# Performance work log

Measured on AMD Instinct MI355X. Metric: run time of the kernel, lower is better.

## Reference

```python
import jax, jax.numpy as jnp
import numpy as np

N_EMBED = 1024
HEAD_SIZE = 64


def setup_inputs() -> dict:
    key = jax.random.key(0)
    kx, kk, kq, kv = jax.random.split(key, 4)
    B, T = 8, 2048
    x = jax.random.normal(kx, (B, T, N_EMBED), dtype=jnp.float32)
    # nn.Linear weights, stored as (in, out) so projection is x @ W
    s = 1.0 / np.sqrt(N_EMBED)
    Wk = jax.random.uniform(kk, (N_EMBED, HEAD_SIZE), jnp.float32, -s, s)
    Wq = jax.random.uniform(kq, (N_EMBED, HEAD_SIZE), jnp.float32, -s, s)
    Wv = jax.random.uniform(kv, (N_EMBED, HEAD_SIZE), jnp.float32, -s, s)
    return {"x": x, "Wk": Wk, "Wq": Wq, "Wv": Wv}


def reference(x, Wk, Wq, Wv):
    # x: [B, T, C] with C = n_embed
    C = x.shape[-1]
    k = x @ Wk  # [B, T, H]
    q = x @ Wq  # [B, T, H]
    v = x @ Wv  # [B, T, H]
    # NOTE: original scales by n_embed**-0.5, not head_size**-0.5
    wei = jnp.einsum("bth,bsh->bts", q, k) * (C ** -0.5)  # [B, T, T]
    wei = jax.nn.softmax(wei, axis=-1)
    # dropout = 0.0 (eval mode) -> identity
    out = jnp.einsum("bts,bsh->bth", wei, v)  # [B, T, H]
    return out
```

## Files before the change

kernel.cpp:

```cpp
#include <hip/hip_runtime.h>
#include <stdint.h>


#define B_ 8
#define T_ 2048
#define C_ 1024
#define H_ 64

typedef float f32x4 __attribute__((ext_vector_type(4)));
typedef short s16x8 __attribute__((ext_vector_type(8)));

__device__ __forceinline__ unsigned int rhu16(float f) {
    return (__float_as_uint(f) + 0x8000u) >> 16;
}
__device__ __forceinline__ unsigned int pkbf(float lo, float hi) {
    unsigned int a = __float_as_uint(lo) + 0x8000u;
    unsigned int b = __float_as_uint(hi) + 0x8000u;
    return __builtin_amdgcn_perm(b, a, 0x07060302u);
}

__global__ __launch_bounds__(256) void wconv(const float* __restrict__ Wk,
        const float* __restrict__ Wq, const float* __restrict__ Wv,
        unsigned short* __restrict__ Wt) {
    int col = blockIdx.x;
    int mat = col >> 6, h = col & 63;
    const float* W = (mat == 0) ? Wk : ((mat == 1) ? Wq : Wv);
    float sc = (mat == 1) ? 0.03125f : 1.0f;
    for (int c = threadIdx.x; c < C_; c += 256)
        Wt[col * C_ + c] = (unsigned short)rhu16(W[c * H_ + h] * sc);
}

__global__ __launch_bounds__(256, 2) void qkv(const float* __restrict__ x,
        const unsigned short* __restrict__ Wt,
        unsigned short* __restrict__ kb, unsigned short* __restrict__ qb,
        unsigned short* __restrict__ vtb) {
    __shared__ unsigned short Ws[192 * 72];

    const int t = threadIdx.x, lane = t & 63, w = t >> 6;
    const int l15 = lane & 15, quad = lane >> 4;
    const int bx = blockIdx.x;
    const int bb = bx >> 6;
    const int mt = ((bx & 7) << 3) | ((bx >> 3) & 7);
    const int m0 = bb * T_ + mt * 32;
    const int colb = w * 48;

    f32x4 acc[2][3];
    #pragma unroll
    for (int rt = 0; rt < 2; rt++)
        #pragma unroll
        for (int ct = 0; ct < 3; ct++)
            #pragma unroll
            for (int j = 0; j < 4; j++) acc[rt][ct][j] = 0.0f;

    for (int c0 = 0; c0 < C_; c0 += 64) {
        __syncthreads();
        #pragma unroll
        for (int u0 = 0; u0 < 6; u0++) {
            int u = t + (u0 << 8);
            int cl = u >> 3, co = (u & 7) << 3;
            uint4 d = *reinterpret_cast<const uint4*>(&Wt[cl * C_ + c0 + co]);
            *reinterpret_cast<uint4*>(&Ws[cl * 72 + co]) = d;
        }
        __syncthreads();
        s16x8 af[2][2];
        #pragma unroll
        for (int rt = 0; rt < 2; rt++)
            #pragma unroll
            for (int ks = 0; ks < 2; ks++) {
                const float* xp = &x[(size_t)(m0 + rt * 16 + l15) * C_ + c0 + ks * 32 + quad * 8];
                float4 a = *reinterpret_cast<const float4*>(xp);
                float4 b = *reinterpret_cast<const float4*>(xp + 4);
                uint4 pk;
                pk.x = pkbf(a.x, a.y); pk.y = pkbf(a.z, a.w);
                pk.z = pkbf(b.x, b.y); pk.w = pkbf(b.z, b.w);
                af[rt][ks] = *reinterpret_cast<s16x8*>(&pk);
            }
        #pragma unroll
        for (int ks = 0; ks < 2; ks++) {
            s16x8 bfr[3];
            #pragma unroll
            for (int ct = 0; ct < 3; ct++)
                bfr[ct] = *reinterpret_cast<const s16x8*>(
                    &Ws[(colb + ct * 16 + l15) * 72 + ks * 32 + quad * 8]);
            #pragma unroll
            for (int rt = 0; rt < 2; rt++)
                #pragma unroll
                for (int ct = 0; ct < 3; ct++)
                    acc[rt][ct] = __builtin_amdgcn_mfma_f32_16x16x32_bf16(
                        af[rt][ks], bfr[ct], acc[rt][ct], 0, 0, 0);
        }
    }
    #pragma unroll
    for (int ct = 0; ct < 3; ct++) {
        int cb = colb + ct * 16;
        int sel = cb >> 6;
        int h = (cb & 63) + l15;
        #pragma unroll
        for (int rt = 0; rt < 2; rt++) {
            int row0 = m0 + rt * 16 + quad * 4;
            if (sel < 2) {
                unsigned short* dst = sel ? qb : kb;
                #pragma unroll
                for (int r = 0; r < 4; r++)
                    dst[(size_t)(row0 + r) * H_ + h] = (unsigned short)rhu16(acc[rt][ct][r]);
            } else {
                int tt = row0 - bb * T_;
                uint2 pk;
                pk.x = pkbf(acc[rt][ct][0], acc[rt][ct][1]);
                pk.y = pkbf(acc[rt][ct][2], acc[rt][ct][3]);
                *reinterpret_cast<uint2*>(&vtb[((size_t)bb * H_ + h) * T_ + tt]) = pk;
            }
        }
    }
}

__global__ __launch_bounds__(256, 2) void attn(
        const unsigned short* __restrict__ qb,
        const unsigned short* __restrict__ kb,
        const unsigned short* __restrict__ vtb,
        float* __restrict__ out) {
    __shared__ float smemf[6432];

    const int t = threadIdx.x, lane = t & 63, w = t >> 6;
    const int l15 = lane & 15, quad = lane >> 4;
    const int bb = blockIdx.x & 7;
    const int q0 = (blockIdx.x >> 3) << 5;
    const size_t kbase = (size_t)bb * T_ * H_;
    unsigned short* Pw = (unsigned short*)smemf + w * 32 * 72;

    s16x8 qf[2][2];
    #pragma unroll
    for (int rt = 0; rt < 2; rt++)
        #pragma unroll
        for (int ks = 0; ks < 2; ks++)
            qf[rt][ks] = *reinterpret_cast<const s16x8*>(
                &qb[kbase + (size_t)(q0 + rt * 16 + l15) * H_ + ks * 32 + quad * 8]);

    f32x4 oacc[2][4];
    #pragma unroll
    for (int rt = 0; rt < 2; rt++)
        #pragma unroll
        for (int ht = 0; ht < 4; ht++)
            #pragma unroll
            for (int j = 0; j < 4; j++) oacc[rt][ht][j] = 0.0f;
    float l_run[2] = {0.0f, 0.0f};
    const f32x4 z4 = {0.0f, 0.0f, 0.0f, 0.0f};

    for (int it = 0; it < 8; it++) {
        const int s0 = (w << 9) + (it << 6);
        s16x8 kf[4][2], vf[2][4];
        #pragma unroll
        for (int st = 0; st < 4; st++)
            #pragma unroll
            for (int ks = 0; ks < 2; ks++)
                kf[st][ks] = *reinterpret_cast<const s16x8*>(
                    &kb[kbase + (size_t)(s0 + st * 16 + l15) * H_ + ks * 32 + quad * 8]);
        #pragma unroll
        for (int ks = 0; ks < 2; ks++)
            #pragma unroll
            for (int ht = 0; ht < 4; ht++)
                vf[ks][ht] = *reinterpret_cast<const s16x8*>(
                    &vtb[((size_t)bb * H_ + ht * 16 + l15) * T_ + s0 + ks * 32 + quad * 8]);

        f32x4 sacc[2][4];
        #pragma unroll
        for (int rt = 0; rt < 2; rt++)
            #pragma unroll
            for (int st = 0; st < 4; st++) {
                f32x4 s = __builtin_amdgcn_mfma_f32_16x16x32_bf16(kf[st][0], qf[rt][0], z4, 0, 0, 0);
                sacc[rt][st] = __builtin_amdgcn_mfma_f32_16x16x32_bf16(kf[st][1], qf[rt][1], s, 0, 0, 0);
            }

        #pragma unroll
        for (int rt = 0; rt < 2; rt++) {
            float ls = 0.0f;
            #pragma unroll
            for (int st = 0; st < 4; st++) {
                float p0 = __expf(sacc[rt][st][0]);
                float p1 = __expf(sacc[rt][st][1]);
                float p2 = __expf(sacc[rt][st][2]);
                float p3 = __expf(sacc[rt][st][3]);
                ls += (p0 + p1) + (p2 + p3);
                uint2 pk;
                pk.x = pkbf(p0, p1);
                pk.y = pkbf(p2, p3);
                *reinterpret_cast<uint2*>(&Pw[(rt * 16 + l15) * 72 + st * 16 + quad * 4]) = pk;
            }
            l_run[rt] += ls;
        }

        #pragma unroll
        for (int rt = 0; rt < 2; rt++)
            #pragma unroll
            for (int ks = 0; ks < 2; ks++) {
                s16x8 pf = *reinterpret_cast<const s16x8*>(
                    &Pw[(rt * 16 + l15) * 72 + ks * 32 + quad * 8]);
                #pragma unroll
                for (int ht = 0; ht < 4; ht++)
                    oacc[rt][ht] = __builtin_amdgcn_mfma_f32_16x16x32_bf16(
                        pf, vf[ks][ht], oacc[rt][ht], 0, 0, 0);
            }
    }

    #pragma unroll
    for (int rt = 0; rt < 2; rt++) {
        l_run[rt] += __shfl_xor(l_run[rt], 16);
        l_run[rt] += __shfl_xor(l_run[rt], 32);
    }

    __syncthreads();
    float* Osf = smemf;
    float* Ls  = smemf + 3 * 32 * 66;
    if (w > 0) {
        int wi = w - 1;
        #pragma unroll
        for (int rt = 0; rt < 2; rt++) {
            if (quad == 0) Ls[wi * 32 + rt * 16 + l15] = l_run[rt];
            #pragma unroll
            for (int ht = 0; ht < 4; ht++)
                #pragma unroll
                for (int r = 0; r < 4; r++)
                    Osf[wi * 2112 + (rt * 16 + quad * 4 + r) * 66 + ht * 16 + l15] = oacc[rt][ht][r];
        }
    }
    __syncthreads();
    if (w == 0) {
        #pragma unroll
        for (int rt = 0; rt < 2; rt++)
            #pragma unroll
            for (int r = 0; r < 4; r++) {
                int row = rt * 16 + quad * 4 + r;
                float lt = __shfl(l_run[rt], quad * 4 + r)
                         + Ls[0 * 32 + row] + Ls[1 * 32 + row] + Ls[2 * 32 + row];
                float inv = 1.0f / lt;
                #pragma unroll
                for (int ht = 0; ht < 4; ht++) {
                    float o = oacc[rt][ht][r]
                            + Osf[0 * 2112 + row * 66 + ht * 16 + l15]
                            + Osf[1 * 2112 + row * 66 + ht * 16 + l15]
                            + Osf[2 * 2112 + row * 66 + ht * 16 + l15];
                    out[kbase + (size_t)(q0 + row) * H_ + ht * 16 + l15] = o * inv;
                }
            }
    }
}

extern "C" void kernel_launch(void* const* d_in, const int* in_sizes, int n_in,
                              void* d_out, int out_size, void* d_ws, size_t ws_size,
                              hipStream_t stream) {
    const float* x  = (const float*)d_in[0];
    const float* Wk = (const float*)d_in[1];
    const float* Wq = (const float*)d_in[2];
    const float* Wv = (const float*)d_in[3];

    unsigned short* kb  = (unsigned short*)d_ws;
    unsigned short* qbf = kb  + (size_t)B_ * T_ * H_;
    unsigned short* vtb = qbf + (size_t)B_ * T_ * H_;
    unsigned short* Wt  = (unsigned short*)d_out;

    wconv<<<192, 256, 0, stream>>>(Wk, Wq, Wv, Wt);
    qkv  <<<512, 256, 0, stream>>>(x, Wt, kb, qbf, vtb);
    attn <<<512, 256, 0, stream>>>(qbf, kb, vtb, (float*)d_out);
}
```

Before: 165.9 us.

## Drop LDS staging in QKV projection, register double-buffer global loads

The QKV projection kernel no longer stages the bf16 weight tile through shared memory with two barriers per K-step. Each wave now loads its own weight fragments and x fragments straight from global memory into registers. The K loop is fully unrolled with a two-slot register buffer so the next step's loads are issued before the current step's MFMAs. This removes the sync and LDS traffic and overlaps memory latency with compute, at the cost of higher register pressure and redundant weight reads across waves and blocks, which now rely on cache.

New measurement: 191.5 us. +15.4%, slower.

```diff
diff --git a/kernel.cpp b/kernel.cpp
--- a/kernel.cpp
+++ b/kernel.cpp
@@ -34,8 +34,6 @@
         const unsigned short* __restrict__ Wt,
         unsigned short* __restrict__ kb, unsigned short* __restrict__ qb,
         unsigned short* __restrict__ vtb) {
-    __shared__ unsigned short Ws[192 * 72];
-
     const int t = threadIdx.x, lane = t & 63, w = t >> 6;
     const int l15 = lane & 15, quad = lane >> 4;
     const int bx = blockIdx.x;
@@ -44,6 +42,15 @@
     const int m0 = bb * T_ + mt * 32;
     const int colb = w * 48;
 
+    const float* xp[2];
+    #pragma unroll
+    for (int rt = 0; rt < 2; rt++)
+        xp[rt] = &x[(size_t)(m0 + rt * 16 + l15) * C_ + quad * 8];
+    const unsigned short* wp[3];
+    #pragma unroll
+    for (int ct = 0; ct < 3; ct++)
+        wp[ct] = &Wt[(size_t)(colb + ct * 16 + l15) * C_ + quad * 8];
+
     f32x4 acc[2][3];
     #pragma unroll
     for (int rt = 0; rt < 2; rt++)
@@ -52,44 +59,64 @@
             #pragma unroll
             for (int j = 0; j < 4; j++) acc[rt][ct][j] = 0.0f;
 
-    for (int c0 = 0; c0 < C_; c0 += 64) {
-        __syncthreads();
-        #pragma unroll
-        for (int u0 = 0; u0 < 6; u0++) {
-            int u = t + (u0 << 8);
-            int cl = u >> 3, co = (u & 7) << 3;
-            uint4 d = *reinterpret_cast<const uint4*>(&Wt[cl * C_ + c0 + co]);
-            *reinterpret_cast<uint4*>(&Ws[cl * 72 + co]) = d;
-        }
-        __syncthreads();
+    float4 xr[2][2][4];
+    uint4  wr[2][3][2];
+
+    #pragma unroll
+    for (int rt = 0; rt < 2; rt++) {
+        xr[0][rt][0] = *reinterpret_cast<const float4*>(xp[rt] + 0);
+        xr[0][rt][1] = *reinterpret_cast<const float4*>(xp[rt] + 4);
+        xr[0][rt][2] = *reinterpret_cast<const float4*>(xp[rt] + 32);
+        xr[0][rt][3] = *reinterpret_cast<const float4*>(xp[rt] + 36);
+    }
+    #pragma unroll
+    for (int ct = 0; ct < 3; ct++) {
+        wr[0][ct][0] = *reinterpret_cast<const uint4*>(wp[ct] + 0);
+        wr[0][ct][1] = *reinterpret_cast<const uint4*>(wp[ct] + 32);
+    }
+
+    #pragma unroll
+    for (int i = 0; i < 16; i++) {
+        const int cur = i & 1, nxt = cur ^ 1;
+        if (i < 15) {
+            const int c1 = (i + 1) * 64;
+            #pragma unroll
+            for (int rt = 0; rt < 2; rt++) {
+                xr[nxt][rt][0] = *reinterpret_cast<const float4*>(xp[rt] + c1 + 0);
+                xr[nxt][rt][1] = *reinterpret_cast<const float4*>(xp[rt] + c1 + 4);
+                xr[nxt][rt][2] = *reinterpret_cast<const float4*>(xp[rt] + c1 + 32);
+                xr[nxt][rt][3] = *reinterpret_cast<const float4*>(xp[rt] + c1 + 36);
+            }
+            #pragma unroll
+            for (int ct = 0; ct < 3; ct++) {
+                wr[nxt][ct][0] = *reinterpret_cast<const uint4*>(wp[ct] + c1 + 0);
+                wr[nxt][ct][1] = *reinterpret_cast<const uint4*>(wp[ct] + c1 + 32);
+            }
+        }
         s16x8 af[2][2];
         #pragma unroll
         for (int rt = 0; rt < 2; rt++)
             #pragma unroll
             for (int ks = 0; ks < 2; ks++) {
-                const float* xp = &x[(size_t)(m0 + rt * 16 + l15) * C_ + c0 + ks * 32 + quad * 8];
-                float4 a = *reinterpret_cast<const float4*>(xp);
-                float4 b = *reinterpret_cast<const float4*>(xp + 4);
+                const float4 a = xr[cur][rt][ks * 2 + 0];
+                const float4 b = xr[cur][rt][ks * 2 + 1];
                 uint4 pk;
                 pk.x = pkbf(a.x, a.y); pk.y = pkbf(a.z, a.w);
                 pk.z = pkbf(b.x, b.y); pk.w = pkbf(b.z, b.w);
                 af[rt][ks] = *reinterpret_cast<s16x8*>(&pk);
             }
         #pragma unroll
-        for (int ks = 0; ks < 2; ks++) {
-            s16x8 bfr[3];
-            #pragma unroll
-            for (int ct = 0; ct < 3; ct++)
-                bfr[ct] = *reinterpret_cast<const s16x8*>(
-                    &Ws[(colb + ct * 16 + l15) * 72 + ks * 32 + quad * 8]);
+        for (int ks = 0; ks < 2; ks++)
             #pragma unroll
             for (int rt = 0; rt < 2; rt++)
                 #pragma unroll
                 for (int ct = 0; ct < 3; ct++)
                     acc[rt][ct] = __builtin_amdgcn_mfma_f32_16x16x32_bf16(
-                        af[rt][ks], bfr[ct], acc[rt][ct], 0, 0, 0);
-        }
-    }
+                        af[rt][ks],
+                        *reinterpret_cast<s16x8*>(&wr[cur][ct][ks]),
+                        acc[rt][ct], 0, 0, 0);
+    }
+
     #pragma unroll
     for (int ct = 0; ct < 3; ct++) {
         int cb = colb + ct * 16;
```

## Double-buffer qkv and attention operands via direct global-to-LDS async loads

Applied to the files above, without the earlier changes.

The qkv kernel now stages both x tiles and weight tiles into double-buffered LDS with global_load_lds, prefetching the next K-chunk while computing the current one. The attention kernel gives each wave its own double-buffered LDS region for K and V tiles in 32-key steps, loaded asynchronously, instead of direct global register loads. The wconv transpose is rewritten to use an LDS tile with coalesced float4 reads and packed writes. The goal is to hide global memory latency, at the cost of much larger LDS use (64KB and 74KB per block), which may reduce occupancy, plus a hand-coded waitcnt.

After: 153.3 us. 7.6% less time.

```diff
diff --git a/kernel.cpp b/kernel.cpp
--- a/kernel.cpp
+++ b/kernel.cpp
@@ -18,23 +18,47 @@
     unsigned int b = __float_as_uint(hi) + 0x8000u;
     return __builtin_amdgcn_perm(b, a, 0x07060302u);
 }
+__device__ __forceinline__ void ld_lds16(const void* g, void* l) {
+    __builtin_amdgcn_global_load_lds(
+        (const __attribute__((address_space(1))) unsigned int*)g,
+        (__attribute__((address_space(3))) unsigned int*)l, 16, 0, 0);
+}
 
 __global__ __launch_bounds__(256) void wconv(const float* __restrict__ Wk,
         const float* __restrict__ Wq, const float* __restrict__ Wv,
         unsigned short* __restrict__ Wt) {
-    int col = blockIdx.x;
-    int mat = col >> 6, h = col & 63;
+    __shared__ float ls[64 * 65];
+    const int bx = blockIdx.x, t = threadIdx.x;
+    const int mat = bx >> 4, c0 = (bx & 15) << 6;
     const float* W = (mat == 0) ? Wk : ((mat == 1) ? Wq : Wv);
-    float sc = (mat == 1) ? 0.03125f : 1.0f;
-    for (int c = threadIdx.x; c < C_; c += 256)
-        Wt[col * C_ + c] = (unsigned short)rhu16(W[c * H_ + h] * sc);
+    const float sc = (mat == 1) ? 0.03125f : 1.0f;
+    #pragma unroll
+    for (int k = 0; k < 4; k++) {
+        int i = t + (k << 8);
+        int cr = i >> 4, hq = (i & 15) << 2;
+        float4 v = *reinterpret_cast<const float4*>(&W[(size_t)(c0 + cr) * H_ + hq]);
+        ls[cr * 65 + hq + 0] = v.x; ls[cr * 65 + hq + 1] = v.y;
+        ls[cr * 65 + hq + 2] = v.z; ls[cr * 65 + hq + 3] = v.w;
+    }
+    __syncthreads();
+    #pragma unroll
+    for (int k = 0; k < 4; k++) {
+        int i = t + (k << 8);
+        int h = i >> 4, cq = (i & 15) << 2;
+        float a = ls[(cq + 0) * 65 + h] * sc, b = ls[(cq + 1) * 65 + h] * sc;
+        float c = ls[(cq + 2) * 65 + h] * sc, d = ls[(cq + 3) * 65 + h] * sc;
+        uint2 o; o.x = pkbf(a, b); o.y = pkbf(c, d);
+        *reinterpret_cast<uint2*>(&Wt[(size_t)(mat * 64 + h) * C_ + c0 + cq]) = o;
+    }
 }
 
 __global__ __launch_bounds__(256, 2) void qkv(const float* __restrict__ x,
         const unsigned short* __restrict__ Wt,
         unsigned short* __restrict__ kb, unsigned short* __restrict__ qb,
         unsigned short* __restrict__ vtb) {
-    __shared__ unsigned short Ws[192 * 72];
+    __shared__ __align__(16) char smem[65536];
+    char* xb = smem;
+    char* wb = smem + 16384;
 
     const int t = threadIdx.x, lane = t & 63, w = t >> 6;
     const int l15 = lane & 15, quad = lane >> 4;
@@ -44,6 +68,27 @@
     const int m0 = bb * T_ + mt * 32;
     const int colb = w * 48;
 
+    size_t xg[2]; int xl[2];
+    #pragma unroll
+    for (int n = 0; n < 2; n++) {
+        int id = w * 2 + n, rg = id >> 2, j = id & 3;
+        xg[n] = (size_t)(m0 + rg * 16 + l15) * C_ + j * 16 + quad * 4;
+        xl[n] = id * 1024 + lane * 16;
+    }
+    size_t wg[6]; int wl[6];
+    #pragma unroll
+    for (int n = 0; n < 6; n++) {
+        int g = w * 6 + n;
+        wg[n] = (size_t)(g * 8 + (lane & 7)) * C_ + (lane >> 3) * 8;
+        wl[n] = g * 1024 + lane * 16;
+    }
+
+    #pragma unroll
+    for (int n = 0; n < 2; n++) ld_lds16(x + xg[n], xb + xl[n]);
+    #pragma unroll
+    for (int n = 0; n < 6; n++) ld_lds16(Wt + wg[n], wb + wl[n]);
+    __syncthreads();
+
     f32x4 acc[2][3];
     #pragma unroll
     for (int rt = 0; rt < 2; rt++)
@@ -52,49 +97,71 @@
             #pragma unroll
             for (int j = 0; j < 4; j++) acc[rt][ct][j] = 0.0f;
 
-    for (int c0 = 0; c0 < C_; c0 += 64) {
-        __syncthreads();
-        #pragma unroll
-        for (int u0 = 0; u0 < 6; u0++) {
-            int u = t + (u0 << 8);
-            int cl = u >> 3, co = (u & 7) << 3;
-            uint4 d = *reinterpret_cast<const uint4*>(&Wt[cl * C_ + c0 + co]);
-            *reinterpret_cast<uint4*>(&Ws[cl * 72 + co]) = d;
-        }
-        __syncthreads();
+    #pragma unroll
+    for (int i = 0; i < 16; i++) {
+        const int cb = i & 1;
+        const float* xc = (const float*)(xb + cb * 8192);
+        const unsigned short* wc = (const unsigned short*)(wb + cb * 24576);
+
+        float4 xr[2][2][2];
+        #pragma unroll
+        for (int rt = 0; rt < 2; rt++)
+            #pragma unroll
+            for (int ks = 0; ks < 2; ks++)
+                #pragma unroll
+                for (int h = 0; h < 2; h++) {
+                    int c = ks * 32 + quad * 8 + h * 4;
+                    int j = c >> 4, u = (c & 15) >> 2;
+                    xr[rt][ks][h] = *reinterpret_cast<const float4*>(
+                        xc + (rt * 4 + j) * 256 + u * 64 + l15 * 4);
+                }
+        s16x8 wfr[3][2];
+        #pragma unroll
+        for (int ct = 0; ct < 3; ct++)
+            #pragma unroll
+            for (int ks = 0; ks < 2; ks++) {
+                int col = colb + ct * 16 + l15;
+                wfr[ct][ks] = *reinterpret_cast<const s16x8*>(
+                    wc + (col >> 3) * 512 + ((4 * ks + quad) * 8 + (col & 7)) * 8);
+            }
+
+        if (i < 15) {
+            const int c1 = (i + 1) * 64;
+            char* xn = xb + (cb ^ 1) * 8192;
+            char* wn = wb + (cb ^ 1) * 24576;
+            #pragma unroll
+            for (int n = 0; n < 2; n++) ld_lds16(x + xg[n] + c1, xn + xl[n]);
+            #pragma unroll
+            for (int n = 0; n < 6; n++) ld_lds16(Wt + wg[n] + c1, wn + wl[n]);
+        }
+
         s16x8 af[2][2];
         #pragma unroll
         for (int rt = 0; rt < 2; rt++)
             #pragma unroll
             for (int ks = 0; ks < 2; ks++) {
-                const float* xp = &x[(size_t)(m0 + rt * 16 + l15) * C_ + c0 + ks * 32 + quad * 8];
-                float4 a = *reinterpret_cast<const float4*>(xp);
-                float4 b = *reinterpret_cast<const float4*>(xp + 4);
+                const float4 a = xr[rt][ks][0], b = xr[rt][ks][1];
                 uint4 pk;
                 pk.x = pkbf(a.x, a.y); pk.y = pkbf(a.z, a.w);
                 pk.z = pkbf(b.x, b.y); pk.w = pkbf(b.z, b.w);
                 af[rt][ks] = *reinterpret_cast<s16x8*>(&pk);
             }
         #pragma unroll
-        for (int ks = 0; ks < 2; ks++) {
-            s16x8 bfr[3];
-            #pragma unroll
-            for (int ct = 0; ct < 3; ct++)
-                bfr[ct] = *reinterpret_cast<const s16x8*>(
-                    &Ws[(colb + ct * 16 + l15) * 72 + ks * 32 + quad * 8]);
+        for (int ks = 0; ks < 2; ks++)
             #pragma unroll
             for (int rt = 0; rt < 2; rt++)
                 #pragma unroll
                 for (int ct = 0; ct < 3; ct++)
                     acc[rt][ct] = __builtin_amdgcn_mfma_f32_16x16x32_bf16(
-                        af[rt][ks], bfr[ct], acc[rt][ct], 0, 0, 0);
-        }
-    }
+                        af[rt][ks], wfr[ct][ks], acc[rt][ct], 0, 0, 0);
+        __syncthreads();
+    }
+
     #pragma unroll
     for (int ct = 0; ct < 3; ct++) {
-        int cb = colb + ct * 16;
-        int sel = cb >> 6;
-        int h = (cb & 63) + l15;
+        int cbv = colb + ct * 16;
+        int sel = cbv >> 6;
+        int h = (cbv & 63) + l15;
         #pragma unroll
         for (int rt = 0; rt < 2; rt++) {
             int row0 = m0 + rt * 16 + quad * 4;
@@ -119,14 +186,16 @@
         const unsigned short* __restrict__ kb,
         const unsigned short* __restrict__ vtb,
         float* __restrict__ out) {
-    __shared__ float smemf[6432];
+    __shared__ __align__(16) char smem[75776];
 
     const int t = threadIdx.x, lane = t & 63, w = t >> 6;
     const int l15 = lane & 15, quad = lane >> 4;
     const int bb = blockIdx.x & 7;
     const int q0 = (blockIdx.x >> 3) << 5;
     const size_t kbase = (size_t)bb * T_ * H_;
-    unsigned short* Pw = (unsigned short*)smemf + w * 32 * 72;
+    char* Kb = smem + w * 16384;
+    char* Vb = Kb + 8192;
+    unsigned short* Pw = (unsigned short*)(smem + 65536 + w * 2560);
 
     s16x8 qf[2][2];
     #pragma unroll
@@ -136,6 +205,23 @@
             qf[rt][ks] = *reinterpret_cast<const s16x8*>(
                 &qb[kbase + (size_t)(q0 + rt * 16 + l15) * H_ + ks * 32 + quad * 8]);
 
+    const unsigned short* kp = kb + kbase;
+    const unsigned short* vp = vtb + (size_t)bb * H_ * T_;
+    size_t kg[4], vg[4]; int kl[4], vl[4];
+    #pragma unroll
+    for (int g = 0; g < 4; g++) {
+        kg[g] = (size_t)(g * 8 + (lane & 7)) * H_ + (lane >> 3) * 8;
+        kl[g] = g * 1024 + lane * 16;
+        vg[g] = (size_t)(g * 16 + l15) * T_ + quad * 8;
+        vl[g] = g * 1024 + lane * 16;
+    }
+
+    const int sw = w << 9;
+    #pragma unroll
+    for (int g = 0; g < 4; g++) ld_lds16(kp + (size_t)sw * H_ + kg[g], Kb + kl[g]);
+    #pragma unroll
+    for (int g = 0; g < 4; g++) ld_lds16(vp + sw + vg[g], Vb + vl[g]);
+
     f32x4 oacc[2][4];
     #pragma unroll
     for (int rt = 0; rt < 2; rt++)
@@ -146,60 +232,70 @@
     float l_run[2] = {0.0f, 0.0f};
     const f32x4 z4 = {0.0f, 0.0f, 0.0f, 0.0f};
 
-    for (int it = 0; it < 8; it++) {
-        const int s0 = (w << 9) + (it << 6);
-        s16x8 kf[4][2], vf[2][4];
-        #pragma unroll
-        for (int st = 0; st < 4; st++)
-            #pragma unroll
-            for (int ks = 0; ks < 2; ks++)
+    for (int it = 0; it < 16; it++) {
+        const int cb = it & 1;
+        __builtin_amdgcn_s_waitcnt(0x0f70);
+        const unsigned short* Kc = (const unsigned short*)(Kb + cb * 4096);
+        const unsigned short* Vc = (const unsigned short*)(Vb + cb * 4096);
+
+        s16x8 kf[2][2], vf[4];
+        #pragma unroll
+        for (int st = 0; st < 2; st++)
+            #pragma unroll
+            for (int ks = 0; ks < 2; ks++) {
+                int s = st * 16 + l15;
                 kf[st][ks] = *reinterpret_cast<const s16x8*>(
-                    &kb[kbase + (size_t)(s0 + st * 16 + l15) * H_ + ks * 32 + quad * 8]);
-        #pragma unroll
-        for (int ks = 0; ks < 2; ks++)
-            #pragma unroll
-            for (int ht = 0; ht < 4; ht++)
-                vf[ks][ht] = *reinterpret_cast<const s16x8*>(
-                    &vtb[((size_t)bb * H_ + ht * 16 + l15) * T_ + s0 + ks * 32 + quad * 8]);
-
-        f32x4 sacc[2][4];
+                    Kc + (s >> 3) * 512 + ((4 * ks + quad) * 8 + (s & 7)) * 8);
+            }
+        #pragma unroll
+        for (int ht = 0; ht < 4; ht++)
+            vf[ht] = *reinterpret_cast<const s16x8*>(
+                Vc + ht * 512 + (quad * 16 + l15) * 8);
+
+        if (it < 15) {
+            const int sn = sw + (it + 1) * 32;
+            char* Kn = Kb + (cb ^ 1) * 4096;
+            char* Vn = Vb + (cb ^ 1) * 4096;
+            #pragma unroll
+            for (int g = 0; g < 4; g++) ld_lds16(kp + (size_t)sn * H_ + kg[g], Kn + kl[g]);
+            #pragma unroll
+            for (int g = 0; g < 4; g++) ld_lds16(vp + sn + vg[g], Vn + vl[g]);
+        }
+
+        f32x4 sacc[2][2];
         #pragma unroll
         for (int rt = 0; rt < 2; rt++)
             #pragma unroll
-            for (int st = 0; st < 4; st++) {
-                f32x4 s = __builtin_amdgcn_mfma_f32_16x16x32_bf16(kf[st][0], qf[rt][0], z4, 0, 0, 0);
-                sacc[rt][st] = __builtin_amdgcn_mfma_f32_16x16x32_bf16(kf[st][1], qf[rt][1], s, 0, 0, 0);
+            for (int st = 0; st < 2; st++) {
+                f32x4 s0v = __builtin_amdgcn_mfma_f32_16x16x32_bf16(kf[st][0], qf[rt][0], z4, 0, 0, 0);
+                sacc[rt][st] = __builtin_amdgcn_mfma_f32_16x16x32_bf16(kf[st][1], qf[rt][1], s0v, 0, 0, 0);
             }
 
         #pragma unroll
         for (int rt = 0; rt < 2; rt++) {
             float ls = 0.0f;
             #pragma unroll
-            for (int st = 0; st < 4; st++) {
+            for (int st = 0; st < 2; st++) {
                 float p0 = __expf(sacc[rt][st][0]);
                 float p1 = __expf(sacc[rt][st][1]);
                 float p2 = __expf(sacc[rt][st][2]);
                 float p3 = __expf(sacc[rt][st][3]);
                 ls += (p0 + p1) + (p2 + p3);
-                uint2 pk;
-                pk.x = pkbf(p0, p1);
-                pk.y = pkbf(p2, p3);
-                *reinterpret_cast<uint2*>(&Pw[(rt * 16 + l15) * 72 + st * 16 + quad * 4]) = pk;
+                uint2 pk; pk.x = pkbf(p0, p1); pk.y = pkbf(p2, p3);
+                *reinterpret_cast<uint2*>(
+                    &Pw[(rt * 16 + l15) * 40 + st * 16 + quad * 4]) = pk;
             }
             l_run[rt] += ls;
         }
 
         #pragma unroll
-        for (int rt = 0; rt < 2; rt++)
-            #pragma unroll
-            for (int ks = 0; ks < 2; ks++) {
-                s16x8 pf = *reinterpret_cast<const s16x8*>(
-                    &Pw[(rt * 16 + l15) * 72 + ks * 32 + quad * 8]);
-                #pragma unroll
-                for (int ht = 0; ht < 4; ht++)
-                    oacc[rt][ht] = __builtin_amdgcn_mfma_f32_16x16x32_bf16(
-                        pf, vf[ks][ht], oacc[rt][ht], 0, 0, 0);
-            }
+        for (int rt = 0; rt < 2; rt++) {
+            s16x8 pf = *reinterpret_cast<const s16x8*>(&Pw[(rt * 16 + l15) * 40 + quad * 8]);
+            #pragma unroll
+            for (int ht = 0; ht < 4; ht++)
+                oacc[rt][ht] = __builtin_amdgcn_mfma_f32_16x16x32_bf16(
+                    pf, vf[ht], oacc[rt][ht], 0, 0, 0);
+        }
     }
 
     #pragma unroll
@@ -209,8 +305,8 @@
     }
 
     __syncthreads();
-    float* Osf = smemf;
-    float* Ls  = smemf + 3 * 32 * 66;
+    float* Osf = (float*)smem;
+    float* Ls  = (float*)smem + 3 * 32 * 66;
     if (w > 0) {
         int wi = w - 1;
         #pragma unroll
@@ -258,7 +354,7 @@
     unsigned short* vtb = qbf + (size_t)B_ * T_ * H_;
     unsigned short* Wt  = (unsigned short*)d_out;
 
-    wconv<<<192, 256, 0, stream>>>(Wk, Wq, Wv, Wt);
+    wconv<<<48,  256, 0, stream>>>(Wk, Wq, Wv, Wt);
     qkv  <<<512, 256, 0, stream>>>(x, Wt, kb, qbf, vtb);
     attn <<<512, 256, 0, stream>>>(qbf, kb, vtb, (float*)d_out);
 }
```
